# Performance work log

Hardware: AMD Instinct MI355X
Metric: run time of the kernel (lower is better)

Reference implementation:

```python
import jax, jax.numpy as jnp
import numpy as np

BASE_RES = 192          # image_shape = [192, 192]
VIEWS = 128             # radial views
READOUT_OS = 2.0        # readout oversampling
SAMPLES = int(BASE_RES * READOUT_OS)  # 384 samples per spoke


def _radial_traj_and_weights():
    """Linear-ordered full-range 2D radial trajectory + ramp density weights."""
    t = jnp.arange(SAMPLES, dtype=jnp.float32)
    # radius spans [-pi, pi) along each spoke (NUFFT convention)
    r = (t - SAMPLES / 2) / (SAMPLES / 2) * jnp.pi            # [samples]
    theta = jnp.arange(VIEWS, dtype=jnp.float32) * (jnp.pi / VIEWS)  # [views]
    kx = r[None, :] * jnp.cos(theta)[:, None]                 # [views, samples]
    ky = r[None, :] * jnp.sin(theta)[:, None]
    points = jnp.stack([kx, ky], axis=-1).reshape(-1, 2)      # [M, 2]
    # geometric (ramp) density compensation: weight ~ |k| with DC floor
    rho = jnp.abs(r) / jnp.pi                                 # [samples], in [0, 1]
    w = jnp.maximum(rho, 1.0 / SAMPLES)                       # avoid zero at DC
    weights = jnp.broadcast_to(w[None, :], (VIEWS, SAMPLES)).reshape(-1)  # [M]
    return points, weights


def setup_inputs() -> dict:
    key = jax.random.key(0)
    x = jax.random.normal(key, (2, BASE_RES, BASE_RES, 2), dtype=jnp.float32)
    points, weights = _radial_traj_and_weights()
    return {"x": x, "points": points, "weights": weights}


def _nudft_resample(xc, points, weights):
    """Type-2 NUDFT (forward) -> density comp -> type-1 NUDFT (adjoint).

    xc: complex [C, B, H, W]; points: [M, 2] in [-pi, pi); weights: [M].
    The 2D nonuniform DFT phase factorizes per axis: exp(-i(kx*nx + ky*ny)).
    """
    C, B, H, W = xc.shape
    nx = (jnp.arange(H, dtype=jnp.float32) - H // 2)          # grid indices
    ny = (jnp.arange(W, dtype=jnp.float32) - W // 2)
    Ax = jnp.exp(-1j * (points[:, 0:1] * nx[None, :]).astype(jnp.complex64))  # [M, H]
    Ay = jnp.exp(-1j * (points[:, 1:2] * ny[None, :]).astype(jnp.complex64))  # [M, W]
    # type-2: k[m] = sum_{h,w} x[h,w] exp(-i(kx_m h + ky_m w))
    tmp = jnp.einsum('cbhw,mh->cbmw', xc, Ax)                 # [C, B, M, W]
    k = jnp.einsum('cbmw,mw->cbm', tmp, Ay)                   # [C, B, M]
    # density compensation
    k = k * weights.astype(jnp.complex64)
    # type-1 adjoint: img[h,w] = sum_m k[m] exp(+i(kx_m h + ky_m w))
    tmp2 = jnp.einsum('cbm,mh->cbmh', k, jnp.conj(Ax))        # [C, B, M, H]
    img = jnp.einsum('cbmh,mw->cbhw', tmp2, jnp.conj(Ay))     # [C, B, H, W]
    # scale by 1 / num_elements(image_shape)
    return img / jnp.asarray(H * W, dtype=jnp.complex64)


def reference(x, points, weights):
    # inputs [B, H, W, C] -> channels-first [C, B, H, W] (layer's perm)
    rank = x.ndim
    perm = [rank - 1] + list(range(rank - 1))
    xc = jnp.transpose(x, perm).astype(jnp.complex64)
    img = _nudft_resample(xc, points, weights)
    out = jnp.abs(img)                                        # layer dtype is real
    inv_perm = list(range(1, rank)) + [0]
    return jnp.transpose(out, inv_perm)                       # [B, H, W, C]
```

## Files before the change

kernel.cpp:

```cpp
#include <hip/hip_runtime.h>
#include <math.h>


#define HH 192
#define WW 192
#define NVIEWS 128
#define NSAMP 384
#define NPIX (HH*WW)
#define HALFT 193
#define M2 12545
#define M2P 12672
#define KTOT 25344
#define NSPLITK 33

typedef __attribute__((ext_vector_type(8))) short bf16x8;
typedef __attribute__((ext_vector_type(4))) float f32x4;
typedef __attribute__((ext_vector_type(8))) unsigned short u16x8;

__device__ __forceinline__ void rot(float& cr, float& ci, float dr, float di) {
  float nr = cr*dr - ci*di;
  float ni = cr*di + ci*dr;
  cr = nr; ci = ni;
}
__device__ __forceinline__ unsigned short f2b(float f) {
  unsigned int u = __float_as_uint(f);
  u += 0x7fffu + ((u >> 16) & 1u);
  return (unsigned short)(u >> 16);
}
__device__ __forceinline__ float b2f(unsigned short h) {
  return __uint_as_float(((unsigned int)h) << 16);
}

__global__ __launch_bounds__(256) void phase_kernel(
    const float* __restrict__ points, unsigned short* __restrict__ BT,
    unsigned short* __restrict__ CxT, unsigned short* __restrict__ SxT,
    unsigned short* __restrict__ Am) {
  const int v2 = blockIdx.x;
  const int role = blockIdx.y;
  const int t = threadIdx.x;
  if (t >= HALFT) return;
  if (role < 4) {
    const int hsplit = role;
    const float kx = points[(v2*NSAMP + t)*2 + 0];
    const int m2 = v2*HALFT + t;
    const int h0 = hsplit*48;
    float cr, ci; __sincosf(kx*(float)(h0-96), &ci, &cr);
    float dr, di; __sincosf(kx, &di, &dr);
    u16x8 pc, ps;
    for (int j = 0; j < 48; ++j) {
      const int h = h0 + j;
      CxT[(size_t)h*M2P + m2] = f2b(cr);
      SxT[(size_t)h*M2P + m2] = f2b(ci);
      pc[j&7] = f2b(cr); ps[j&7] = f2b(ci);
      if ((j&7) == 7) {
        *(u16x8*)(Am + (size_t)m2*192 + (h-7))         = pc;
        *(u16x8*)(Am + (size_t)(12672+m2)*192 + (h-7)) = ps;
      }
      rot(cr, ci, dr, di);
    }
  } else {
    const int wsplit = role - 4;
    const float ky = points[(v2*NSAMP + t)*2 + 1];
    const int kap = v2*HALFT + t;
    const int w0 = wsplit*48;
    float cr, ci; __sincosf(ky*(float)(w0-96), &ci, &cr);
    float dr, di; __sincosf(ky, &di, &dr);
    for (int j = 0; j < 48; ++j) {
      BT[(size_t)(w0+j)*KTOT + kap]       = f2b(cr);
      BT[(size_t)(w0+j)*KTOT + M2P + kap] = f2b(ci);
      rot(cr, ci, dr, di);
    }
  }
}


__global__ __launch_bounds__(256) void xprep_kernel(
    const float* __restrict__ x, unsigned short* __restrict__ XT) {
  const int idx = blockIdx.x*256 + threadIdx.x;
  if (idx >= 768*192) return;
  const int n = idx / 192, h = idx - n*192;
  const int cb = n / 192, w = n - cb*192;
  const int b = cb >> 1, c = cb & 1;
  XT[idx] = f2b(x[(((size_t)b*HH + h)*WW + w)*2 + c]);
}

__global__ __launch_bounds__(256) void gemm1_kernel(
    const unsigned short* __restrict__ Am, const unsigned short* __restrict__ XT,
    const float* __restrict__ points, float* __restrict__ Abuf) {
  __shared__ float lds[2][128][2];
  const int mt = blockIdx.x;
  const int cb = blockIdx.y;
  const int wv = threadIdx.x >> 6;
  const int lane = threadIdx.x & 63;
  const int r = lane & 15, kg = lane >> 4;
  const int mhalf = wv >> 1;
  const int whalf = wv & 1;
  const int mbase = mt*128 + mhalf*64;
  const int wbase = whalf*96;
  const int nbase = cb*192 + wbase;

  f32x4 acc[4][6];
  #pragma unroll
  for (int a = 0; a < 4; ++a)
    #pragma unroll
    for (int b = 0; b < 6; ++b) acc[a][b] = (f32x4){0.f,0.f,0.f,0.f};

  const unsigned short* Ap = Am + (size_t)(mbase + r)*192 + kg*8;
  const unsigned short* Bp = XT + (size_t)(nbase + r)*192 + kg*8;
  #pragma unroll
  for (int ks = 0; ks < 6; ++ks) {
    bf16x8 af[4], bfr[6];
    #pragma unroll
    for (int mf = 0; mf < 4; ++mf)
      af[mf] = *(const bf16x8*)(Ap + (size_t)mf*16*192 + ks*32);
    #pragma unroll
    for (int nf = 0; nf < 6; ++nf)
      bfr[nf] = *(const bf16x8*)(Bp + (size_t)nf*16*192 + ks*32);
    #pragma unroll
    for (int mf = 0; mf < 4; ++mf)
      #pragma unroll
      for (int nf = 0; nf < 6; ++nf)
        acc[mf][nf] = __builtin_amdgcn_mfma_f32_16x16x32_bf16(
            af[mf], bfr[nf], acc[mf][nf], 0, 0, 0);
  }

  const bool isCx = (mt < 99);
  const int m2w = mbase - (isCx ? 0 : 12672);
  float accA[16], accB[16];
  #pragma unroll
  for (int mf = 0; mf < 4; ++mf)
    #pragma unroll
    for (int reg = 0; reg < 4; ++reg) {
      const int m2 = m2w + mf*16 + kg*4 + reg;
      const int v2 = m2 / HALFT, t = m2 - v2*HALFT;
      const float ky = points[(v2*NSAMP + t)*2 + 1];
      float a0 = 0.f, b0 = 0.f;
      #pragma unroll
      for (int nf = 0; nf < 6; ++nf) {
        const float wo = (float)(wbase + nf*16 + r - 96);
        float sy, cy; __sincosf(ky*wo, &sy, &cy);
        const float g = acc[mf][nf][reg];
        a0 = fmaf(g, cy, a0);
        b0 = fmaf(g, sy, b0);
      }
      accA[mf*4+reg] = a0; accB[mf*4+reg] = b0;
    }
  #pragma unroll
  for (int msk = 1; msk <= 8; msk <<= 1) {
    #pragma unroll
    for (int i = 0; i < 16; ++i) {
      accA[i] += __shfl_xor(accA[i], msk);
      accB[i] += __shfl_xor(accB[i], msk);
    }
  }
  if (r == 0) {
    #pragma unroll
    for (int mf = 0; mf < 4; ++mf)
      #pragma unroll
      for (int reg = 0; reg < 4; ++reg) {
        const int mloc = mhalf*64 + mf*16 + kg*4 + reg;
        lds[whalf][mloc][0] = accA[mf*4+reg];
        lds[whalf][mloc][1] = accB[mf*4+reg];
      }
  }
  __syncthreads();
  {
    const int tid = threadIdx.x;
    const int mloc = tid >> 1, slot = tid & 1;
    const float val = lds[0][mloc][slot] + lds[1][mloc][slot];
    const int m2 = mt*128 + mloc - (isCx ? 0 : 12672);
    const int idx = isCx ? (slot ? 3 : 0) : (slot ? 1 : 2);
    Abuf[((size_t)cb*M2P + m2)*4 + idx] = val;
  }
}

__global__ __launch_bounds__(256) void combine2_kernel(
    const float* __restrict__ Abuf, const float* __restrict__ weights,
    float* __restrict__ combos, float* __restrict__ K2edge) {
  const int m2 = blockIdx.x*256 + threadIdx.x;
  if (m2 >= M2) return;
  const int v2 = m2 / HALFT, t = m2 - v2*HALFT;
  float f = weights[t] * (1.0f/36864.0f);
  if (t != 0 && t != 192) f *= 2.0f;
  const bool hp = (v2 >= 1 && v2 <= 63);
  #pragma unroll
  for (int cb = 0; cb < 4; ++cb) {
    const float4 A = *(const float4*)(Abuf + ((size_t)cb*M2P + m2)*4);
    const float A1 = A.x, A2 = A.y, A3 = A.z, A4 = A.w;
    float c0, c1, c2, c3;
    if (hp) {
      c0 =  2.f*f*A1; c1 = -2.f*f*A2; c2 = -2.f*f*A4; c3 = -2.f*f*A3;
    } else {
      const float kr = f*(A1 - A2), ki = -f*(A3 + A4);
      c0 = kr; c1 = kr; c2 = ki; c3 = ki;
    }
    combos[(cb*4+0)*M2P + m2] = c0;
    combos[(cb*4+1)*M2P + m2] = c1;
    combos[(cb*4+2)*M2P + m2] = c2;
    combos[(cb*4+3)*M2P + m2] = c3;
    if (t == 0 || t == 192) {
      const int d = (t == 0) ? 0 : 1;
      float* e = K2edge + ((v2*2 + d)*4 + cb)*2;
      e[0] = f*(A1 - A2); e[1] = -f*(A3 + A4);
      if (hp) {
        float* e2 = K2edge + (((128 - v2)*2 + d)*4 + cb)*2;
        e2[0] = f*(A1 + A2); e2[1] = f*(A3 - A4);
      }
    }
  }
}


__global__ __launch_bounds__(256) void tmat_kernel(
    const float* __restrict__ combos, const unsigned short* __restrict__ CxT,
    const unsigned short* __restrict__ SxT, unsigned short* __restrict__ A) {
  const int m2 = blockIdx.x*256 + threadIdx.x;
  if (m2 >= M2P) return;
  const int j = blockIdx.y;
  unsigned short* Arow = A + (size_t)j*KTOT;
  if (m2 >= M2) { Arow[m2] = 0; Arow[M2P + m2] = 0; return; }
  const int cb = j / 192, h = j - cb*192;
  const float cx = b2f(CxT[(size_t)h*M2P + m2]);
  const float sx = b2f(SxT[(size_t)h*M2P + m2]);
  const float c0 = combos[(cb*4+0)*M2P + m2];
  const float c1 = combos[(cb*4+1)*M2P + m2];
  const float c2 = combos[(cb*4+2)*M2P + m2];
  const float c3 = combos[(cb*4+3)*M2P + m2];
  Arow[m2]       = f2b(c0*cx - c3*sx);
  Arow[M2P + m2] = f2b(-(c1*sx + c2*cx));
}

__global__ __launch_bounds__(256) void adj_gemm(
    const unsigned short* __restrict__ A, const unsigned short* __restrict__ BT,
    float* __restrict__ partials) {
  const int mt = blockIdx.x;
  const int kc = blockIdx.y;
  const int wv = threadIdx.x >> 6;
  const int lane = threadIdx.x & 63;
  const int r = lane & 15, kg = lane >> 4;
  const int jbase = mt*128 + (wv>>1)*64;
  const int wbase = (wv&1)*96;
  const int kb = kc*768 + kg*8;

  f32x4 acc[4][6];
  #pragma unroll
  for (int a = 0; a < 4; ++a)
    #pragma unroll
    for (int b = 0; b < 6; ++b) acc[a][b] = (f32x4){0.f,0.f,0.f,0.f};

  const unsigned short* Ap = A + (size_t)(jbase + r)*KTOT + kb;
  const unsigned short* Bp = BT + (size_t)(wbase + r)*KTOT + kb;
  for (int ks = 0; ks < 24; ++ks) {
    bf16x8 af[4], bfr[6];
    #pragma unroll
    for (int mf = 0; mf < 4; ++mf)
      af[mf] = *(const bf16x8*)(Ap + (size_t)mf*16*KTOT + ks*32);
    #pragma unroll
    for (int nf = 0; nf < 6; ++nf)
      bfr[nf] = *(const bf16x8*)(Bp + (size_t)nf*16*KTOT + ks*32);
    #pragma unroll
    for (int mf = 0; mf < 4; ++mf)
      #pragma unroll
      for (int nf = 0; nf < 6; ++nf)
        acc[mf][nf] = __builtin_amdgcn_mfma_f32_16x16x32_bf16(
            af[mf], bfr[nf], acc[mf][nf], 0, 0, 0);
  }
  float* base = partials + (size_t)kc*192*768;
  #pragma unroll
  for (int mf = 0; mf < 4; ++mf)
    #pragma unroll
    for (int nf = 0; nf < 6; ++nf) {
      const int w = wbase + nf*16 + r;
      const int j = jbase + mf*16 + kg*4;
      *(f32x4*)(base + (size_t)w*768 + j) = acc[mf][nf];
    }
}

__global__ __launch_bounds__(256) void im_kernel(
    const unsigned short* __restrict__ BT, const unsigned short* __restrict__ CxT,
    const unsigned short* __restrict__ SxT, const float* __restrict__ K2edge,
    float* __restrict__ imb) {
  __shared__ float cxs[65][8], sxs[65][8], cys[65][8], sys[65][8];
  __shared__ float red[4][64][4];
  const int bx = blockIdx.x;
  const int h0 = (bx/24)*8, w0 = (bx%24)*8;
  const int tid = threadIdx.x;
  for (int i = tid; i < 65*8; i += 256) {
    const int v2 = i >> 3, e = i & 7;
    const int kap = v2*HALFT;
    cxs[v2][e] = b2f(CxT[(size_t)(h0+e)*M2P + kap]);
    sxs[v2][e] = b2f(SxT[(size_t)(h0+e)*M2P + kap]);
    cys[v2][e] = b2f(BT[(size_t)(w0+e)*KTOT + kap]);
    sys[v2][e] = b2f(BT[(size_t)(w0+e)*KTOT + M2P + kap]);
  }
  __syncthreads();
  const int g = tid >> 6, hi = (tid >> 3) & 7, wi = tid & 7;
  float im[4] = {0,0,0,0};
  for (int v = g*32; v < g*32 + 32; ++v) {
    const int v2 = (v <= 64) ? v : 128 - v;
    const float sg = (v <= 64) ? 1.f : -1.f;
    const float cx = cxs[v2][hi], sx = sg*sxs[v2][hi];
    const float cy = cys[v2][wi], sy = sys[v2][wi];
    const float t1 = cx*sy + sx*cy;
    const float t2 = cx*cy - sx*sy;
    const int idx = v*16;
    #pragma unroll
    for (int cb = 0; cb < 4; ++cb)
      im[cb] += K2edge[idx + cb*2]*t1 + K2edge[idx + cb*2 + 1]*t2;
  }
  const int p = tid & 63;
  #pragma unroll
  for (int cb = 0; cb < 4; ++cb) red[g][p][cb] = im[cb];
  __syncthreads();
  if (g == 0) {
    #pragma unroll
    for (int cb = 0; cb < 4; ++cb)
      im[cb] += red[1][p][cb] + red[2][p][cb] + red[3][p][cb];
    const int pix = (h0+hi)*192 + (w0+wi);
    *(float4*)(imb + pix*4) = make_float4(im[0], im[1], im[2], im[3]);
  }
}

__global__ __launch_bounds__(256) void out_new_kernel(
    const float* __restrict__ partials, const float* __restrict__ imb,
    float* __restrict__ out) {
  const int g = blockIdx.x*256 + threadIdx.x;
  const int w = g / 768, cbh = g - w*768;
  const int cb = cbh / 192, h = cbh - cb*192;
  float re = 0.f;
  for (int kc = 0; kc < NSPLITK; ++kc)
    re += partials[(size_t)kc*147456 + g];
  const float im = imb[(h*192 + w)*4 + cb];
  const float mag = sqrtf(re*re + im*im);
  const int b = cb >> 1, c = cb & 1;
  out[((size_t)b*NPIX + h*192 + w)*2 + c] = mag;
}


template <int HPER>
__global__ __launch_bounds__(192) void fwd_kernel(
    const float* __restrict__ x, const float* __restrict__ points,
    float* __restrict__ kpart) {
  const int v = blockIdx.x;
  const int split = blockIdx.y;
  const int t = threadIdx.x;
  const int m = v*NSAMP + t;
  const float kx = points[2*m+0];
  const float ky = points[2*m+1];
  const int h0 = split*HPER;

  float kr[4] = {0,0,0,0}, ki[4] = {0,0,0,0};
  float cyr, cyi; __sincosf(96.0f*ky, &cyi, &cyr);
  float dyr, dyi; __sincosf(-ky, &dyi, &dyr);
  float cx0r, cx0i; __sincosf(kx*(float)(96-h0), &cx0i, &cx0r);
  float dxr, dxi; __sincosf(-kx, &dxi, &dxr);

  for (int wp = 0; wp < 96; ++wp) {
    const int w0 = wp*2;
    float g0r[4]={0,0,0,0}, g0i[4]={0,0,0,0};
    float g1r[4]={0,0,0,0}, g1i[4]={0,0,0,0};
    float cxr = cx0r, cxi = cx0i;
    const float* p0 = x + (h0*WW + w0)*2;
    const float* p1 = p0 + HH*WW*2;
    #pragma unroll 4
    for (int h = 0; h < HPER; ++h) {
      float4 a = *(const float4*)(p0 + h*(WW*2));
      float4 b = *(const float4*)(p1 + h*(WW*2));
      g0r[0] += a.x*cxr; g0i[0] += a.x*cxi;
      g0r[1] += a.y*cxr; g0i[1] += a.y*cxi;
      g1r[0] += a.z*cxr; g1i[0] += a.z*cxi;
      g1r[1] += a.w*cxr; g1i[1] += a.w*cxi;
      g0r[2] += b.x*cxr; g0i[2] += b.x*cxi;
      g0r[3] += b.y*cxr; g0i[3] += b.y*cxi;
      g1r[2] += b.z*cxr; g1i[2] += b.z*cxi;
      g1r[3] += b.w*cxr; g1i[3] += b.w*cxi;
      rot(cxr, cxi, dxr, dxi);
    }
    #pragma unroll
    for (int cb = 0; cb < 4; ++cb) {
      kr[cb] += g0r[cb]*cyr - g0i[cb]*cyi;
      ki[cb] += g0r[cb]*cyi + g0i[cb]*cyr;
    }
    rot(cyr, cyi, dyr, dyi);
    #pragma unroll
    for (int cb = 0; cb < 4; ++cb) {
      kr[cb] += g1r[cb]*cyr - g1i[cb]*cyi;
      ki[cb] += g1r[cb]*cyi + g1i[cb]*cyr;
    }
    rot(cyr, cyi, dyr, dyi);
  }
  float* o = kpart + (((split*NVIEWS + v)*192 + t)*4)*2;
  #pragma unroll
  for (int cb = 0; cb < 4; ++cb) { o[2*cb] = kr[cb]; o[2*cb+1] = ki[cb]; }
}

__global__ __launch_bounds__(256) void dc_kernel(
    const float* __restrict__ x, float* __restrict__ dcsum) {
  const int tid = threadIdx.x;
  float s0=0.f, s1=0.f, s2=0.f, s3=0.f;
  for (int i = tid; i < NPIX; i += 256) {
    float2 a = *(const float2*)(x + i*2);
    float2 b = *(const float2*)(x + HH*WW*2 + i*2);
    s0 += a.x; s1 += a.y; s2 += b.x; s3 += b.y;
  }
  #pragma unroll
  for (int off = 32; off > 0; off >>= 1) {
    s0 += __shfl_down(s0, off);
    s1 += __shfl_down(s1, off);
    s2 += __shfl_down(s2, off);
    s3 += __shfl_down(s3, off);
  }
  __shared__ float red[4][4];
  const int wv = tid >> 6, ln = tid & 63;
  if (ln == 0) { red[0][wv]=s0; red[1][wv]=s1; red[2][wv]=s2; red[3][wv]=s3; }
  __syncthreads();
  if (tid < 4) {
    float tot = red[tid][0]+red[tid][1]+red[tid][2]+red[tid][3];
    dcsum[2*tid] = tot; dcsum[2*tid+1] = 0.0f;
  }
}

__global__ __launch_bounds__(256) void combine_kernel(
    const float* __restrict__ kpart, const float* __restrict__ dcsum,
    const float* __restrict__ weights, float* __restrict__ K2, int nsplit) {
  const int idx = blockIdx.x*256 + threadIdx.x;
  if (idx >= NVIEWS*HALFT) return;
  const int v = idx / HALFT, t = idx % HALFT;
  float f = weights[t] * (1.0f/36864.0f);
  if (t != 0 && t != 192) f *= 2.0f;
  float o[8];
  if (t == 192) {
    #pragma unroll
    for (int cb = 0; cb < 4; ++cb) { o[2*cb] = f*dcsum[2*cb]; o[2*cb+1] = f*dcsum[2*cb+1]; }
  } else {
    #pragma unroll
    for (int cb = 0; cb < 4; ++cb) {
      float ar = 0.f, ai = 0.f;
      for (int s = 0; s < nsplit; ++s) {
        const float* p = kpart + (((s*NVIEWS + v)*192 + t)*4 + cb)*2;
        ar += p[0]; ai += p[1];
      }
      o[2*cb] = f*ar; o[2*cb+1] = f*ai;
    }
  }
  float* q = K2 + idx*8;
  #pragma unroll
  for (int j = 0; j < 8; ++j) q[j] = o[j];
}

template <int VPC>
__global__ __launch_bounds__(256) void adj_kernel(
    const float* __restrict__ K2, const float* __restrict__ points,
    float* __restrict__ imgpart) {
  const int pix = blockIdx.x*256 + threadIdx.x;
  const int chunk = blockIdx.y;
  const float nh = (float)(pix / WW - 96);
  const float nw = (float)(pix % WW - 96);
  float re[4] = {0,0,0,0}, im[4] = {0,0,0,0};
  const float INVPI = 0.3183098861837907f;
  const float PI192 = 3.14159265358979f / 192.0f;
  for (int v = chunk*VPC; v < chunk*VPC + VPC; ++v) {
    const float ct = -points[2*(v*NSAMP)+0] * INVPI;
    const float st = -points[2*(v*NSAMP)+1] * INVPI;
    const float alpha = ct*nh + st*nw;
    const float delta = alpha * PI192;
    float dr, di; __sincosf(delta, &di, &dr);
    float c0r, c0i; __sincosf(-192.0f*delta, &c0i, &c0r);
    const float* Kv = K2 + v*HALFT*8;
    #pragma unroll
    for (int cb = 0; cb < 4; ++cb) {
      float a = Kv[2*cb], b = Kv[2*cb+1];
      re[cb] += a*c0r - b*c0i;
      im[cb] += a*c0i + b*c0r;
    }
    float d2r = dr*dr - di*di, d2i = 2.0f*dr*di;
    float ar = c0r*dr - c0i*di, ai = c0r*di + c0i*dr;
    float br = ar*dr - ai*di,  bi = ar*di + ai*dr;
    for (int i = 0; i < 95; ++i) {
      const float* ka = Kv + (2*i+1)*8;
      const float* kb = Kv + (2*i+2)*8;
      #pragma unroll
      for (int cb = 0; cb < 4; ++cb)
        re[cb] += ka[2*cb]*ar - ka[2*cb+1]*ai;
      #pragma unroll
      for (int cb = 0; cb < 4; ++cb)
        re[cb] += kb[2*cb]*br - kb[2*cb+1]*bi;
      rot(ar, ai, d2r, d2i);
      rot(br, bi, d2r, d2i);
    }
    {
      const float* ka = Kv + 191*8;
      #pragma unroll
      for (int cb = 0; cb < 4; ++cb)
        re[cb] += ka[2*cb]*ar - ka[2*cb+1]*ai;
    }
    const float* kd = Kv + 192*8;
    #pragma unroll
    for (int cb = 0; cb < 4; ++cb) { re[cb] += kd[2*cb]; im[cb] += kd[2*cb+1]; }
  }
  float* o = imgpart + (chunk*NPIX + pix)*8;
  #pragma unroll
  for (int cb = 0; cb < 4; ++cb) { o[2*cb] = re[cb]; o[2*cb+1] = im[cb]; }
}

__global__ __launch_bounds__(256) void out_fb_kernel(
    const float* __restrict__ imgpart, float* __restrict__ out, int nchunk) {
  const int pix = blockIdx.x*256 + threadIdx.x;
  float re[4] = {0,0,0,0}, im[4] = {0,0,0,0};
  for (int ch = 0; ch < nchunk; ++ch) {
    const float* p = imgpart + (ch*NPIX + pix)*8;
    #pragma unroll
    for (int cb = 0; cb < 4; ++cb) { re[cb] += p[2*cb]; im[cb] += p[2*cb+1]; }
  }
  #pragma unroll
  for (int b = 0; b < 2; ++b)
    #pragma unroll
    for (int c = 0; c < 2; ++c) {
      const int cb = b*2 + c;
      out[(b*NPIX + pix)*2 + c] = sqrtf(re[cb]*re[cb] + im[cb]*im[cb]);
    }
}

extern "C" void kernel_launch(void* const* d_in, const int* in_sizes, int n_in,
                              void* d_out, int out_size, void* d_ws, size_t ws_size,
                              hipStream_t stream) {
  const float* x       = (const float*)d_in[0];
  const float* points  = (const float*)d_in[1];
  const float* weights = (const float*)d_in[2];
  float* out = (float*)d_out;

  const size_t NEED = 79265792ull;
  if (ws_size >= NEED) {
    char* wsb = (char*)d_ws;
    unsigned short* BT   = (unsigned short*)(wsb + 0);
    unsigned short* CxT  = (unsigned short*)(wsb + 9732096);
    unsigned short* SxT  = (unsigned short*)(wsb + 14598144);
    float* combos        = (float*)(wsb + 19464192);
    float* K2edge        = (float*)(wsb + 20275200);
    char* S              = wsb + 20283392;
    unsigned short* Am   = (unsigned short*)(S + 0);
    unsigned short* XT   = (unsigned short*)(S + 9732096);
    float* Abuf          = (float*)(S + 10027008);
    unsigned short* Aadj = (unsigned short*)(S + 0);
    float* partials      = (float*)(S + 38928384);
    float* imb           = (float*)(S + 58392576);

    phase_kernel<<<dim3(65,8), 256, 0, stream>>>(points, BT, CxT, SxT, Am);
    xprep_kernel<<<576, 256, 0, stream>>>(x, XT);
    gemm1_kernel<<<dim3(198,4), 256, 0, stream>>>(Am, XT, points, Abuf);
    combine2_kernel<<<(M2 + 255)/256, 256, 0, stream>>>(
        Abuf, weights, combos, K2edge);
    tmat_kernel<<<dim3((M2P + 255)/256, 768), 256, 0, stream>>>(
        combos, CxT, SxT, Aadj);
    adj_gemm<<<dim3(6, NSPLITK), 256, 0, stream>>>(Aadj, BT, partials);
    im_kernel<<<576, 256, 0, stream>>>(BT, CxT, SxT, K2edge, imb);
    out_new_kernel<<<(192*768)/256, 256, 0, stream>>>(partials, imb, out);
  } else {
    float* ws = (float*)d_ws;
    const size_t ws_floats = ws_size / sizeof(float);
    int nsplit = 16, nchunk = 16;
    auto need = [&](int ns, int nc) -> size_t {
      return (size_t)ns*196608 + 8 + 197632 + (size_t)nc*294912;
    };
    while (need(nsplit, nchunk) > ws_floats && nchunk > 1) nchunk >>= 1;
    while (need(nsplit, nchunk) > ws_floats && nsplit > 1) nsplit >>= 1;

    float* kpart   = ws;
    float* dcsum   = kpart + (size_t)nsplit*196608;
    float* K2      = dcsum + 8;
    float* imgpart = K2 + 197632;

    switch (nsplit) {
      case 16: fwd_kernel<12><<<dim3(NVIEWS,16), 192, 0, stream>>>(x, points, kpart); break;
      case 8:  fwd_kernel<24><<<dim3(NVIEWS,8),  192, 0, stream>>>(x, points, kpart); break;
      case 4:  fwd_kernel<48><<<dim3(NVIEWS,4),  192, 0, stream>>>(x, points, kpart); break;
      case 2:  fwd_kernel<96><<<dim3(NVIEWS,2),  192, 0, stream>>>(x, points, kpart); break;
      default: fwd_kernel<192><<<dim3(NVIEWS,1), 192, 0, stream>>>(x, points, kpart); break;
    }
    dc_kernel<<<1, 256, 0, stream>>>(x, dcsum);
    combine_kernel<<<(NVIEWS*HALFT + 255)/256, 256, 0, stream>>>(
        kpart, dcsum, weights, K2, nsplit);
    switch (nchunk) {
      case 16: adj_kernel<8>  <<<dim3(NPIX/256,16), 256, 0, stream>>>(K2, points, imgpart); break;
      case 8:  adj_kernel<16> <<<dim3(NPIX/256,8),  256, 0, stream>>>(K2, points, imgpart); break;
      case 4:  adj_kernel<32> <<<dim3(NPIX/256,4),  256, 0, stream>>>(K2, points, imgpart); break;
      case 2:  adj_kernel<64> <<<dim3(NPIX/256,2),  256, 0, stream>>>(K2, points, imgpart); break;
      default: adj_kernel<128><<<dim3(NPIX/256,1),  256, 0, stream>>>(K2, points, imgpart); break;
    }
    out_fb_kernel<<<NPIX/256, 256, 0, stream>>>(imgpart, out, nchunk);
  }
}
```

Before: 137.3 us.

## Fold input prep into phase kernel, reuse phase loads in tmat, remap adj_gemm to XCDs

The standalone xprep kernel becomes an extra grid row inside phase_kernel, which removes one launch. The tmat kernel now loops over the four channel-batch slices per h, so each Cx/Sx phase load is reused four times. To allow that, combine2 pre-signs its coefficients and zero-fills the padded entries. adj_gemm switches to a 1D grid that maps split-K chunks to XCDs (L&7), so blocks sharing a K chunk stay on one XCD for L2 locality. This adds 240-198=42 early-exit blocks.

```diff
diff --git a/kernel.cpp b/kernel.cpp
--- a/kernel.cpp
+++ b/kernel.cpp
@@ -32,12 +32,22 @@
 }
 
 __global__ __launch_bounds__(256) void phase_kernel(
-    const float* __restrict__ points, unsigned short* __restrict__ BT,
-    unsigned short* __restrict__ CxT, unsigned short* __restrict__ SxT,
-    unsigned short* __restrict__ Am) {
+    const float* __restrict__ points, const float* __restrict__ x,
+    unsigned short* __restrict__ BT, unsigned short* __restrict__ CxT,
+    unsigned short* __restrict__ SxT, unsigned short* __restrict__ Am,
+    unsigned short* __restrict__ XT) {
   const int v2 = blockIdx.x;
   const int role = blockIdx.y;
   const int t = threadIdx.x;
+  if (role == 8) {
+    for (int idx = v2*256 + t; idx < 768*192; idx += 65*256) {
+      const int n = idx / 192, h = idx - n*192;
+      const int cb = n / 192, w = n - cb*192;
+      const int b = cb >> 1, c = cb & 1;
+      XT[idx] = f2b(x[(((size_t)b*HH + h)*WW + w)*2 + c]);
+    }
+    return;
+  }
   if (t >= HALFT) return;
   if (role < 4) {
     const int hsplit = role;
@@ -74,16 +84,6 @@
 }
 
 
-__global__ __launch_bounds__(256) void xprep_kernel(
-    const float* __restrict__ x, unsigned short* __restrict__ XT) {
-  const int idx = blockIdx.x*256 + threadIdx.x;
-  if (idx >= 768*192) return;
-  const int n = idx / 192, h = idx - n*192;
-  const int cb = n / 192, w = n - cb*192;
-  const int b = cb >> 1, c = cb & 1;
-  XT[idx] = f2b(x[(((size_t)b*HH + h)*WW + w)*2 + c]);
-}
-
 __global__ __launch_bounds__(256) void gemm1_kernel(
     const unsigned short* __restrict__ Am, const unsigned short* __restrict__ XT,
     const float* __restrict__ points, float* __restrict__ Abuf) {
@@ -178,7 +178,12 @@
     const float* __restrict__ Abuf, const float* __restrict__ weights,
     float* __restrict__ combos, float* __restrict__ K2edge) {
   const int m2 = blockIdx.x*256 + threadIdx.x;
-  if (m2 >= M2) return;
+  if (m2 >= M2P) return;
+  if (m2 >= M2) {
+    #pragma unroll
+    for (int q = 0; q < 16; ++q) combos[(size_t)q*M2P + m2] = 0.f;
+    return;
+  }
   const int v2 = m2 / HALFT, t = m2 - v2*HALFT;
   float f = weights[t] * (1.0f/36864.0f);
   if (t != 0 && t != 192) f *= 2.0f;
@@ -187,17 +192,17 @@
   for (int cb = 0; cb < 4; ++cb) {
     const float4 A = *(const float4*)(Abuf + ((size_t)cb*M2P + m2)*4);
     const float A1 = A.x, A2 = A.y, A3 = A.z, A4 = A.w;
-    float c0, c1, c2, c3;
+    float p0, p1, q0, q1;
     if (hp) {
-      c0 =  2.f*f*A1; c1 = -2.f*f*A2; c2 = -2.f*f*A4; c3 = -2.f*f*A3;
+      p0 = 2.f*f*A1; p1 = 2.f*f*A3; q0 = 2.f*f*A4; q1 = 2.f*f*A2;
     } else {
       const float kr = f*(A1 - A2), ki = -f*(A3 + A4);
-      c0 = kr; c1 = kr; c2 = ki; c3 = ki;
-    }
-    combos[(cb*4+0)*M2P + m2] = c0;
-    combos[(cb*4+1)*M2P + m2] = c1;
-    combos[(cb*4+2)*M2P + m2] = c2;
-    combos[(cb*4+3)*M2P + m2] = c3;
+      p0 = kr; p1 = -ki; q0 = -ki; q1 = -kr;
+    }
+    combos[(size_t)(cb*4+0)*M2P + m2] = p0;
+    combos[(size_t)(cb*4+1)*M2P + m2] = p1;
+    combos[(size_t)(cb*4+2)*M2P + m2] = q0;
+    combos[(size_t)(cb*4+3)*M2P + m2] = q1;
     if (t == 0 || t == 192) {
       const int d = (t == 0) ? 0 : 1;
       float* e = K2edge + ((v2*2 + d)*4 + cb)*2;
@@ -216,25 +221,30 @@
     const unsigned short* __restrict__ SxT, unsigned short* __restrict__ A) {
   const int m2 = blockIdx.x*256 + threadIdx.x;
   if (m2 >= M2P) return;
-  const int j = blockIdx.y;
-  unsigned short* Arow = A + (size_t)j*KTOT;
-  if (m2 >= M2) { Arow[m2] = 0; Arow[M2P + m2] = 0; return; }
-  const int cb = j / 192, h = j - cb*192;
+  const int h = blockIdx.y;
   const float cx = b2f(CxT[(size_t)h*M2P + m2]);
   const float sx = b2f(SxT[(size_t)h*M2P + m2]);
-  const float c0 = combos[(cb*4+0)*M2P + m2];
-  const float c1 = combos[(cb*4+1)*M2P + m2];
-  const float c2 = combos[(cb*4+2)*M2P + m2];
-  const float c3 = combos[(cb*4+3)*M2P + m2];
-  Arow[m2]       = f2b(c0*cx - c3*sx);
-  Arow[M2P + m2] = f2b(-(c1*sx + c2*cx));
+  #pragma unroll
+  for (int cb = 0; cb < 4; ++cb) {
+    unsigned short* Arow = A + (size_t)(cb*192 + h)*KTOT;
+    const float p0 = combos[(size_t)(cb*4+0)*M2P + m2];
+    const float p1 = combos[(size_t)(cb*4+1)*M2P + m2];
+    const float q0 = combos[(size_t)(cb*4+2)*M2P + m2];
+    const float q1 = combos[(size_t)(cb*4+3)*M2P + m2];
+    Arow[m2]       = f2b(p0*cx + p1*sx);
+    Arow[M2P + m2] = f2b(q0*cx + q1*sx);
+  }
 }
 
 __global__ __launch_bounds__(256) void adj_gemm(
     const unsigned short* __restrict__ A, const unsigned short* __restrict__ BT,
     float* __restrict__ partials) {
-  const int mt = blockIdx.x;
-  const int kc = blockIdx.y;
+  const int L = blockIdx.x;
+  const int xcd = L & 7, slot = L >> 3;
+  const int g = slot / 6;
+  const int kc = g*8 + xcd;
+  if (kc >= NSPLITK) return;
+  const int mt = slot - g*6;
   const int wv = threadIdx.x >> 6;
   const int lane = threadIdx.x & 63;
   const int r = lane & 15, kg = lane >> 4;
@@ -545,14 +555,13 @@
     float* partials      = (float*)(S + 38928384);
     float* imb           = (float*)(S + 58392576);
 
-    phase_kernel<<<dim3(65,8), 256, 0, stream>>>(points, BT, CxT, SxT, Am);
-    xprep_kernel<<<576, 256, 0, stream>>>(x, XT);
+    phase_kernel<<<dim3(65,9), 256, 0, stream>>>(points, x, BT, CxT, SxT, Am, XT);
     gemm1_kernel<<<dim3(198,4), 256, 0, stream>>>(Am, XT, points, Abuf);
-    combine2_kernel<<<(M2 + 255)/256, 256, 0, stream>>>(
+    combine2_kernel<<<(M2P + 255)/256, 256, 0, stream>>>(
         Abuf, weights, combos, K2edge);
-    tmat_kernel<<<dim3((M2P + 255)/256, 768), 256, 0, stream>>>(
+    tmat_kernel<<<dim3((M2P + 255)/256, 192), 256, 0, stream>>>(
         combos, CxT, SxT, Aadj);
-    adj_gemm<<<dim3(6, NSPLITK), 256, 0, stream>>>(Aadj, BT, partials);
+    adj_gemm<<<240, 256, 0, stream>>>(Aadj, BT, partials);
     im_kernel<<<576, 256, 0, stream>>>(BT, CxT, SxT, K2edge, imb);
     out_new_kernel<<<(192*768)/256, 256, 0, stream>>>(partials, imb, out);
   } else {
```

Result: faster. 127.9 us (-6.8%).
